# Performance work log

Measured on AMD Instinct MI355X. Metric: run time of the kernel, lower is better.

## Reference

```python
import jax, jax.numpy as jnp
import numpy as np
from jax import lax

D_MODEL = 256
SCALES = 3
DM2 = 2 * D_MODEL            # 512, inner d_model of each Mamba2
EXPAND = 2
D_INNER = EXPAND * DM2       # 1024
HEADDIM = 64                 # Mamba2 default
NHEADS = D_INNER // HEADDIM  # 16
DSTATE = 128
DCONV = 4
D_IN_PROJ = 2 * D_INNER + 2 * DSTATE + NHEADS  # 2320
CONV_CH = D_INNER + 2 * DSTATE                 # 1280


def layernorm(x, g, b, eps=1e-5):
    mu = x.mean(-1, keepdims=True)
    v = ((x - mu) ** 2).mean(-1, keepdims=True)
    return (x - mu) * lax.rsqrt(v + eps) * g + b


def mamba2(x, Win, convw, convb, dtb, Alog, Dh, normw, Wout):
    # x: [B, L, DM2]
    Bb, L, _ = x.shape
    zxbcdt = x @ Win                                   # [B, L, 2320]
    z = zxbcdt[..., :D_INNER]                          # gate branch
    xBC = zxbcdt[..., D_INNER:D_INNER + CONV_CH]       # [B, L, 1280]
    dt = jax.nn.softplus(zxbcdt[..., -NHEADS:] + dtb)  # [B, L, H]
    # causal depthwise conv1d over time
    xc = lax.conv_general_dilated(
        xBC.transpose(0, 2, 1), convw[:, None, :], (1,), [(DCONV - 1, 0)],
        feature_group_count=CONV_CH, dimension_numbers=('NCH', 'OIH', 'NCH'))
    xBC = jax.nn.silu(xc.transpose(0, 2, 1) + convb)
    xs = xBC[..., :D_INNER].reshape(Bb, L, NHEADS, HEADDIM)  # [B,L,H,P]
    Bm = xBC[..., D_INNER:D_INNER + DSTATE]                  # [B,L,N] (ngroups=1)
    Cm = xBC[..., D_INNER + DSTATE:]                         # [B,L,N]
    A = -jnp.exp(Alog)                                       # [H]
    dA = jnp.exp(dt * A)                                     # [B,L,H]

    def step(h, inp):
        dA_t, dt_t, x_t, B_t, C_t = inp
        h = dA_t[:, :, None, None] * h + jnp.einsum('bh,bhp,bn->bhpn', dt_t, x_t, B_t)
        return h, jnp.einsum('bhpn,bn->bhp', h, C_t)

    h0 = jnp.zeros((Bb, NHEADS, HEADDIM, DSTATE), x.dtype)
    _, ys = lax.scan(step, h0, (dA.transpose(1, 0, 2), dt.transpose(1, 0, 2),
                                xs.transpose(1, 0, 2, 3), Bm.transpose(1, 0, 2),
                                Cm.transpose(1, 0, 2)))
    y = ys.transpose(1, 0, 2, 3) + Dh[None, None, :, None] * xs   # skip term
    y = y.reshape(Bb, L, D_INNER)
    y = y * jax.nn.silu(z)                                        # gated RMSNorm
    y = y * lax.rsqrt((y * y).mean(-1, keepdims=True) + 1e-5) * normw
    return y @ Wout


def msfusion(x, Wp, bp, Wpre, bpre, lnpre_g, lnpre_b, Wpost, bpost, lnpost_g, lnpost_b,
             Win_f, convw_f, convb_f, dtb_f, Alog_f, Dh_f, normw_f, Wout_f,
             Win_b, convw_b, convb_b, dtb_b, Alog_b, Dh_b, normw_b, Wout_b):
    B, S, T, D = x.shape
    x_ = x.transpose(0, 2, 1, 3).reshape(B, T, S * D)
    x_ = x_ @ Wp + bp                                  # 1x1 conv == linear
    shortcut = x_
    h = layernorm(x_ @ Wpre + bpre, lnpre_g, lnpre_b)  # [B,T,512]
    gate = jax.nn.silu(h)
    out_f = mamba2(h, Win_f, convw_f, convb_f, dtb_f, Alog_f, Dh_f, normw_f, Wout_f)
    out_b = jnp.flip(mamba2(jnp.flip(h, 1), Win_b, convw_b, convb_b, dtb_b, Alog_b, Dh_b, normw_b, Wout_b), 1)
    out = layernorm((out_f * gate + out_b * gate) @ Wpost + bpost, lnpost_g, lnpost_b) + shortcut
    fn = out / jnp.maximum(jnp.linalg.norm(out, axis=-1, keepdims=True), 1e-12)
    attn = jnp.einsum('btd,bsd->bts', fn, fn)          # [B,T,T]
    return out, attn


def setup_inputs() -> dict:
    key = jax.random.key(0)
    ks = iter(jax.random.split(key, 40))
    n = lambda shape, s=0.02: (s * jax.random.normal(next(ks), shape)).astype(jnp.float32)
    B, S, T, D = 4, SCALES, 2048, D_MODEL
    inp = {
        'x': jax.random.normal(next(ks), (B, S, T, D), jnp.float32),
        'Wp': n((S * D, D)), 'bp': n((D,)),
        'Wpre': n((D, DM2)), 'bpre': n((DM2,)),
        'lnpre_g': jnp.ones((DM2,), jnp.float32), 'lnpre_b': jnp.zeros((DM2,), jnp.float32),
        'Wpost': n((DM2, D)), 'bpost': n((D,)),
        'lnpost_g': jnp.ones((D,), jnp.float32), 'lnpost_b': jnp.zeros((D,), jnp.float32),
    }
    for sfx in ('f', 'b'):
        inp['Win_' + sfx] = n((DM2, D_IN_PROJ))
        inp['convw_' + sfx] = n((CONV_CH, DCONV), 0.1)
        inp['convb_' + sfx] = jnp.zeros((CONV_CH,), jnp.float32)
        inp['dtb_' + sfx] = n((NHEADS,), 0.5)
        inp['Alog_' + sfx] = jnp.log(jnp.arange(1, NHEADS + 1, dtype=jnp.float32))
        inp['Dh_' + sfx] = jnp.ones((NHEADS,), jnp.float32)
        inp['normw_' + sfx] = jnp.ones((D_INNER,), jnp.float32)
        inp['Wout_' + sfx] = n((D_INNER, DM2))
    return inp


def reference(x, Wp, bp, Wpre, bpre, lnpre_g, lnpre_b, Wpost, bpost, lnpost_g, lnpost_b,
              Win_f, convw_f, convb_f, dtb_f, Alog_f, Dh_f, normw_f, Wout_f,
              Win_b, convw_b, convb_b, dtb_b, Alog_b, Dh_b, normw_b, Wout_b):
    return msfusion(x, Wp, bp, Wpre, bpre, lnpre_g, lnpre_b, Wpost, bpost, lnpost_g, lnpost_b,
                    Win_f, convw_f, convb_f, dtb_f, Alog_f, Dh_f, normw_f, Wout_f,
                    Win_b, convw_b, convb_b, dtb_b, Alog_b, Dh_b, normw_b, Wout_b)
```

## Files before the change

### kernel.cpp

```cpp
#include <hip/hip_runtime.h>
#include <math.h>

__device__ __forceinline__ float sigf(float v) { return 1.f / (1.f + __expf(-v)); }

__device__ __forceinline__ short f2bf(float f) {
  unsigned int u = __builtin_bit_cast(unsigned int, f);
  unsigned int r = (u + 0x7fffu + ((u >> 16) & 1u)) >> 16;
  return (short)r;
}
__device__ __forceinline__ float bf2f(short s) {
  unsigned int u = ((unsigned int)(unsigned short)s) << 16;
  return __builtin_bit_cast(float, u);
}

typedef short bf16x8 __attribute__((ext_vector_type(8)));
typedef float f32x4 __attribute__((ext_vector_type(4)));

__device__ __forceinline__ void async16(const short* g, short* l) {
  __builtin_amdgcn_global_load_lds(
      (const __attribute__((address_space(1))) unsigned int*)g,
      (__attribute__((address_space(3))) unsigned int*)l, 16, 0, 0);
}

template<bool BIAS, bool ACC>
__global__ __launch_bounds__(256) void gemm16_kernel(
    const short* __restrict__ A, const short* __restrict__ Bt,
    const float* __restrict__ bias, float* __restrict__ C,
    int M, int N, int K, int ldc,
    long long sAb, long long sBb, long long sCb)
{
  __shared__ short sm[2][2][128 * 32];
  const int tid = threadIdx.x;
  const int wave = tid >> 6;
  const int lane = tid & 63;
  const int m0 = blockIdx.x * 128;
  const int n0 = blockIdx.y * 128;
  const int bz = blockIdx.z;
  const short* Ab = A + (size_t)bz * sAb;
  const short* Bb = Bt + (size_t)bz * sBb;
  float* Cb = C + (size_t)bz * sCb;

  f32x4 acc[4][4] = {};

  const int isB = wave >> 1;
  const int half = wave & 1;
  const short* gsrc = isB ? Bb : Ab;
  const int tile_r0 = isB ? n0 : m0;
  const int lrow = lane >> 2;
  const int lk = (lane & 3) * 8;
  const short* gbase = gsrc + (size_t)(tile_r0 + half * 64 + lrow) * K + lk;
  short* lbase0 = &sm[0][isB][(half * 64) * 32];
  short* lbase1 = &sm[1][isB][(half * 64) * 32];

  const int wm = wave >> 1, wn = wave & 1;
  const int nt = K >> 5;

  auto STAGE = [&](int buf, int t) {
    const short* g0 = gbase + t * 32;
    short* l0 = buf ? lbase1 : lbase0;
#pragma unroll
    for (int c = 0; c < 4; c++)
      async16(g0 + (size_t)c * 16 * K, l0 + c * 512);
  };

  STAGE(0, 0);
  asm volatile("s_waitcnt vmcnt(0)" ::: "memory");
  __builtin_amdgcn_s_barrier();

  int cur = 0;
  for (int t = 0; t < nt; ++t) {
    if (t + 1 < nt) STAGE(cur ^ 1, t + 1);
    bf16x8 af[4], bfr[4];
#pragma unroll
    for (int mt = 0; mt < 4; mt++)
      af[mt] = *(bf16x8*)&sm[cur][0][(wm * 64 + mt * 16 + (lane & 15)) * 32 + (lane >> 4) * 8];
#pragma unroll
    for (int nn = 0; nn < 4; nn++)
      bfr[nn] = *(bf16x8*)&sm[cur][1][(wn * 64 + nn * 16 + (lane & 15)) * 32 + (lane >> 4) * 8];
#pragma unroll
    for (int mt = 0; mt < 4; mt++)
#pragma unroll
      for (int nn = 0; nn < 4; nn++)
        acc[mt][nn] = __builtin_amdgcn_mfma_f32_16x16x32_bf16(bfr[nn], af[mt], acc[mt][nn], 0, 0, 0);
    asm volatile("s_waitcnt vmcnt(0)" ::: "memory");
    __builtin_amdgcn_s_barrier();
    cur ^= 1;
  }
  const int mcol = lane & 15;
  const int nq = (lane >> 4) * 4;
#pragma unroll
  for (int mt = 0; mt < 4; mt++) {
    int row = m0 + wm * 64 + mt * 16 + mcol;
#pragma unroll
    for (int nn = 0; nn < 4; nn++) {
      int col = n0 + wn * 64 + nn * 16 + nq;
      if (col >= N) continue;
      float4 v = make_float4(acc[mt][nn][0], acc[mt][nn][1], acc[mt][nn][2], acc[mt][nn][3]);
      float* cp = Cb + (size_t)row * ldc + col;
      if (BIAS) {
        float4 bv = *(const float4*)(bias + col);
        v.x += bv.x; v.y += bv.y; v.z += bv.z; v.w += bv.w;
      }
      if (ACC) {
        float4 ov = *(const float4*)cp;
        v.x += ov.x; v.y += ov.y; v.z += ov.z; v.w += ov.w;
      }
      *(float4*)cp = v;
    }
  }
}

__global__ void tcast_kernel(const float* __restrict__ W, short* __restrict__ Wt,
                             int K, int N)
{
  __shared__ float tile[32][33];
  int n0 = blockIdx.x * 32, k0 = blockIdx.y * 32;
  int c = threadIdx.x & 31, r8 = threadIdx.x >> 5;
#pragma unroll
  for (int i = 0; i < 4; i++) {
    int r = r8 + i * 8;
    int n = n0 + c;
    tile[r][c] = (n < N) ? W[(size_t)(k0 + r) * N + n] : 0.f;
  }
  __syncthreads();
#pragma unroll
  for (int i = 0; i < 4; i++) {
    int r = r8 + i * 8;
    Wt[(size_t)(n0 + r) * K + k0 + c] = f2bf(tile[c][r]);
  }
}

__global__ void gather_cast_kernel(const float* __restrict__ x, short* __restrict__ Ag)
{
  int idx = blockIdx.x * 256 + threadIdx.x;
  int m = idx / 192;
  int g = idx - m * 192;
  int k = g * 4;
  int s = k >> 8, d = k & 255;
  int b = m >> 11, t = m & 2047;
  float4 v = *(const float4*)(x + ((size_t)((b * 3 + s) * 2048 + t) << 8) + d);
  *(short4*)(Ag + (size_t)m * 768 + k) = make_short4(f2bf(v.x), f2bf(v.y), f2bf(v.z), f2bf(v.w));
}

__global__ void cast_kernel(const float* __restrict__ in, short* __restrict__ out)
{
  size_t idx = (size_t)blockIdx.x * 256 + threadIdx.x;
  float4 v = *(const float4*)(in + idx * 4);
  *(short4*)(out + idx * 4) = make_short4(f2bf(v.x), f2bf(v.y), f2bf(v.z), f2bf(v.w));
}

__global__ void ln512_kernel(float* __restrict__ xio, const float* __restrict__ g,
                             const float* __restrict__ b, short* __restrict__ o16)
{
  const int row = blockIdx.x;
  const int lane = threadIdx.x;
  float* xr = xio + (size_t)row * 512;
  float4 v0 = *(float4*)(xr + lane * 4);
  float4 v1 = *(float4*)(xr + 256 + lane * 4);
  float sum = v0.x + v0.y + v0.z + v0.w + v1.x + v1.y + v1.z + v1.w;
#pragma unroll
  for (int o = 32; o >= 1; o >>= 1) sum += __shfl_xor(sum, o);
  const float mu = sum * (1.f / 512.f);
  float d[8] = {v0.x - mu, v0.y - mu, v0.z - mu, v0.w - mu,
                v1.x - mu, v1.y - mu, v1.z - mu, v1.w - mu};
  float vs = 0.f;
#pragma unroll
  for (int i = 0; i < 8; i++) vs += d[i] * d[i];
#pragma unroll
  for (int o = 32; o >= 1; o >>= 1) vs += __shfl_xor(vs, o);
  const float inv = rsqrtf(vs * (1.f / 512.f) + 1e-5f);
  float4 g0 = *(const float4*)(g + lane * 4);
  float4 g1 = *(const float4*)(g + 256 + lane * 4);
  float4 b0 = *(const float4*)(b + lane * 4);
  float4 b1 = *(const float4*)(b + 256 + lane * 4);
  v0.x = d[0] * inv * g0.x + b0.x; v0.y = d[1] * inv * g0.y + b0.y;
  v0.z = d[2] * inv * g0.z + b0.z; v0.w = d[3] * inv * g0.w + b0.w;
  v1.x = d[4] * inv * g1.x + b1.x; v1.y = d[5] * inv * g1.y + b1.y;
  v1.z = d[6] * inv * g1.z + b1.z; v1.w = d[7] * inv * g1.w + b1.w;
  *(float4*)(xr + lane * 4) = v0;
  *(float4*)(xr + 256 + lane * 4) = v1;
  short* orow = o16 + (size_t)row * 512;
  *(short4*)(orow + lane * 4) = make_short4(f2bf(v0.x), f2bf(v0.y), f2bf(v0.z), f2bf(v0.w));
  *(short4*)(orow + 256 + lane * 4) = make_short4(f2bf(v1.x), f2bf(v1.y), f2bf(v1.z), f2bf(v1.w));
}

__global__ void dtprep_kernel(const float* __restrict__ Z, const float* __restrict__ dtb,
                              const float* __restrict__ Alog,
                              float* __restrict__ dtv, float* __restrict__ ldA)
{
  int idx = blockIdx.x * 256 + threadIdx.x;
  int row = idx >> 4, hh = idx & 15;
  float raw = Z[(size_t)row * 2320 + 2304 + hh] + dtb[hh];
  float dt = raw > 20.f ? raw : log1pf(expf(raw));
  dtv[idx] = dt;
  ldA[idx] = -dt * expf(Alog[hh]);
}

__global__ void conv_kernel(const float* __restrict__ Z, const float* __restrict__ convw,
                            const float* __restrict__ convb, short* __restrict__ xcv, int dir)
{
  int row = blockIdx.x;
  int c = blockIdx.y * 256 + threadIdx.x;
  int t = row & 2047;
  size_t bbase = (size_t)(row - t) * 2320;
  float wv[4] = {convw[c * 4 + 0], convw[c * 4 + 1], convw[c * 4 + 2], convw[c * 4 + 3]};
  float acc = convb[c];
#pragma unroll
  for (int k = 0; k < 4; k++) {
    int ts = dir ? (t + 3 - k) : (t - 3 + k);
    if (ts >= 0 && ts < 2048)
      acc += wv[k] * Z[bbase + (size_t)ts * 2320 + 1024 + c];
  }
  xcv[(size_t)row * 1280 + c] = f2bf(acc * sigf(acc));
}

__global__ __launch_bounds__(256) void chunk_state_kernel(
    const short* __restrict__ xcv, const float* __restrict__ dtv,
    const float* __restrict__ ldA, short* __restrict__ Sbuf,
    float* __restrict__ Pbuf, int dir)
{
  __shared__ float sw[64];
  __shared__ short sXT[64 * 72];
  __shared__ short sBw[128 * 72];
  const int bh = blockIdx.x, ck = blockIdx.y;
  const int b = bh >> 4, h = bh & 15;
  const int tid = threadIdx.x;
  const int wave = tid >> 6, lane = tid & 63;

  if (tid < 64) {
    int tg = ck * 64 + tid;
    int tt = dir ? 2047 - tg : tg;
    size_t r = (size_t)(b * 2048 + tt) * 16 + h;
    float v = ldA[r];
#pragma unroll
    for (int o = 1; o < 64; o <<= 1) { float u = __shfl_up(v, o); if (tid >= o) v += u; }
    float tot = __shfl(v, 63);
    sw[tid] = __expf(tot - v) * dtv[r];
    if (tid == 63) Pbuf[bh * 32 + ck] = __expf(tot);
  }
  __syncthreads();
  for (int i4 = tid; i4 < 512; i4 += 256) {
    int s = i4 >> 3, p0 = (i4 & 7) * 8;
    int tg = ck * 64 + s; int tt = dir ? 2047 - tg : tg;
    bf16x8 xv = *(const bf16x8*)(xcv + (size_t)(b * 2048 + tt) * 1280 + h * 64 + p0);
#pragma unroll
    for (int j = 0; j < 8; j++) sXT[(p0 + j) * 72 + s] = xv[j];
  }
  for (int i4 = tid; i4 < 1024; i4 += 256) {
    int s = i4 >> 4, n0 = (i4 & 15) * 8;
    int tg = ck * 64 + s; int tt = dir ? 2047 - tg : tg;
    bf16x8 bv = *(const bf16x8*)(xcv + (size_t)(b * 2048 + tt) * 1280 + 1024 + n0);
    float w = sw[s];
#pragma unroll
    for (int j = 0; j < 8; j++) sBw[(n0 + j) * 72 + s] = f2bf(w * bf2f(bv[j]));
  }
  __syncthreads();

  const int mcol = lane & 15, kgrp = (lane >> 4) * 8;
  bf16x8 af[2];
#pragma unroll
  for (int kk = 0; kk < 2; kk++)
    af[kk] = *(bf16x8*)&sXT[(wave * 16 + mcol) * 72 + kk * 32 + kgrp];
  f32x4 acc[8] = {};
#pragma unroll
  for (int j = 0; j < 8; j++)
#pragma unroll
    for (int kk = 0; kk < 2; kk++) {
      bf16x8 bf = *(bf16x8*)&sBw[(j * 16 + mcol) * 72 + kk * 32 + kgrp];
      acc[j] = __builtin_amdgcn_mfma_f32_16x16x32_bf16(bf, af[kk], acc[j], 0, 0, 0);
    }
  short* Sp = Sbuf + ((size_t)(bh * 32 + ck) << 13);
  const int p = wave * 16 + mcol;
  const int nq = (lane >> 4) * 4;
#pragma unroll
  for (int j = 0; j < 8; j++) {
    *(short4*)(Sp + p * 128 + j * 16 + nq) = make_short4(
        f2bf(acc[j][0]), f2bf(acc[j][1]), f2bf(acc[j][2]), f2bf(acc[j][3]));
  }
}

__global__ void chunk_scan_kernel(short* __restrict__ Sbuf, const float* __restrict__ Pbuf)
{
  int idx = blockIdx.x * 256 + threadIdx.x;
  int bh = idx >> 12, pr = idx & 4095;
  float h0 = 0.f, h1 = 0.f;
  for (int ck = 0; ck < 32; ck++) {
    size_t off = ((size_t)(bh * 32 + ck) << 13) + pr * 2;
    unsigned int u = *(const unsigned int*)(Sbuf + off);
    float s0 = bf2f((short)(u & 0xffff));
    float s1 = bf2f((short)(u >> 16));
    float P = Pbuf[bh * 32 + ck];
    unsigned int w = (unsigned int)(unsigned short)f2bf(h0) |
                     ((unsigned int)(unsigned short)f2bf(h1) << 16);
    *(unsigned int*)(Sbuf + off) = w;
    h0 = P * h0 + s0;
    h1 = P * h1 + s1;
  }
}

__global__ __launch_bounds__(256) void chunk_out_kernel(
    const short* __restrict__ xcv, const float* __restrict__ dtv,
    const float* __restrict__ ldA, const short* __restrict__ Sbuf,
    const float* __restrict__ Dh, short* __restrict__ y, int dir)
{
  extern __shared__ short smem16[];
  short* sC  = smem16;
  short* sB  = sC + 64 * 136;
  short* sH  = sB + 64 * 136;
  short* sXT = sH + 64 * 136;
  short* sP  = sXT + 64 * 72;
  float* sL  = (float*)(sP + 64 * 72);
  float* sdt = sL + 64;

  const int bh = blockIdx.x, ck = blockIdx.y;
  const int b = bh >> 4, h = bh & 15;
  const int tid = threadIdx.x;
  const int wave = tid >> 6, lane = tid & 63;

  if (tid < 64) {
    int tg = ck * 64 + tid;
    int tt = dir ? 2047 - tg : tg;
    size_t r = (size_t)(b * 2048 + tt) * 16 + h;
    float v = ldA[r];
#pragma unroll
    for (int o = 1; o < 64; o <<= 1) { float u = __shfl_up(v, o); if (tid >= o) v += u; }
    sL[tid] = v;
    sdt[tid] = dtv[r];
  }
  for (int i4 = tid; i4 < 1024; i4 += 256) {
    int t = i4 >> 4, c8 = (i4 & 15) * 8;
    int tg = ck * 64 + t; int tt = dir ? 2047 - tg : tg;
    const short* rp = xcv + (size_t)(b * 2048 + tt) * 1280;
    *(bf16x8*)&sB[t * 136 + c8] = *(const bf16x8*)(rp + 1024 + c8);
    *(bf16x8*)&sC[t * 136 + c8] = *(const bf16x8*)(rp + 1152 + c8);
  }
  for (int i4 = tid; i4 < 512; i4 += 256) {
    int t = i4 >> 3, p0 = (i4 & 7) * 8;
    int tg = ck * 64 + t; int tt = dir ? 2047 - tg : tg;
    bf16x8 xv = *(const bf16x8*)(xcv + (size_t)(b * 2048 + tt) * 1280 + h * 64 + p0);
#pragma unroll
    for (int j = 0; j < 8; j++) sXT[(p0 + j) * 72 + t] = xv[j];
  }
  const short* Hp = Sbuf + ((size_t)(bh * 32 + ck) << 13);
  for (int i4 = tid; i4 < 1024; i4 += 256) {
    int p = i4 >> 4, c8 = (i4 & 15) * 8;
    *(bf16x8*)&sH[p * 136 + c8] = *(const bf16x8*)(Hp + p * 128 + c8);
  }
  __syncthreads();

  const int mcol = lane & 15;
  const int kgrp = (lane >> 4) * 8;
  const int trow = wave * 16 + mcol;
  const int sq = (lane >> 4) * 4;

  bf16x8 afC[4];
#pragma unroll
  for (int kk = 0; kk < 4; kk++)
    afC[kk] = *(bf16x8*)&sC[trow * 136 + kk * 32 + kgrp];

  f32x4 sacc[4] = {};
#pragma unroll
  for (int j = 0; j < 4; j++)
#pragma unroll
    for (int kk = 0; kk < 4; kk++) {
      bf16x8 bf = *(bf16x8*)&sB[(j * 16 + mcol) * 136 + kk * 32 + kgrp];
      sacc[j] = __builtin_amdgcn_mfma_f32_16x16x32_bf16(bf, afC[kk], sacc[j], 0, 0, 0);
    }

  const float Lt = sL[trow];
#pragma unroll
  for (int j = 0; j < 4; j++) {
    int s0 = j * 16 + sq;
    float vr[4];
#pragma unroll
    for (int r = 0; r < 4; r++) {
      int s = s0 + r;
      vr[r] = (trow >= s) ? sacc[j][r] * __expf(Lt - sL[s]) * sdt[s] : 0.f;
    }
    *(short4*)&sP[trow * 72 + s0] = make_short4(
        f2bf(vr[0]), f2bf(vr[1]), f2bf(vr[2]), f2bf(vr[3]));
  }
  __syncthreads();

  bf16x8 afP[2];
#pragma unroll
  for (int kk = 0; kk < 2; kk++)
    afP[kk] = *(bf16x8*)&sP[trow * 72 + kk * 32 + kgrp];
  f32x4 yacc[4] = {};
#pragma unroll
  for (int j = 0; j < 4; j++)
#pragma unroll
    for (int kk = 0; kk < 2; kk++) {
      bf16x8 bf = *(bf16x8*)&sXT[(j * 16 + mcol) * 72 + kk * 32 + kgrp];
      yacc[j] = __builtin_amdgcn_mfma_f32_16x16x32_bf16(bf, afP[kk], yacc[j], 0, 0, 0);
    }
  f32x4 y2[4] = {};
#pragma unroll
  for (int j = 0; j < 4; j++)
#pragma unroll
    for (int kk = 0; kk < 4; kk++) {
      bf16x8 bf = *(bf16x8*)&sH[(j * 16 + mcol) * 136 + kk * 32 + kgrp];
      y2[j] = __builtin_amdgcn_mfma_f32_16x16x32_bf16(bf, afC[kk], y2[j], 0, 0, 0);
    }

  const float dh = Dh[h];
  const float eL = __expf(Lt);
  const int tg = ck * 64 + trow;
  const int tt = dir ? 2047 - tg : tg;
  short* yrow = y + (size_t)(b * 2048 + tt) * 1024 + h * 64;
#pragma unroll
  for (int j = 0; j < 4; j++) {
    int p0 = j * 16 + sq;
    short o[4];
#pragma unroll
    for (int r = 0; r < 4; r++) {
      float xv = bf2f(sXT[(p0 + r) * 72 + trow]);
      o[r] = f2bf(yacc[j][r] + eL * y2[j][r] + dh * xv);
    }
    *(short4*)(yrow + p0) = make_short4(o[0], o[1], o[2], o[3]);
  }
}

__global__ void rms_kernel(short* __restrict__ y, const float* __restrict__ Z,
                           const float* __restrict__ normw)
{
  const int row = blockIdx.x;
  const int lane = threadIdx.x;
  short* yr = y + (size_t)row * 1024;
  const float* zr = Z + (size_t)row * 2320;
  float vals[16];
  float ss = 0.f;
#pragma unroll
  for (int jj = 0; jj < 4; jj++) {
    int off = jj * 256 + lane * 4;
    short4 yv = *(short4*)(yr + off);
    float4 zv = *(const float4*)(zr + off);
    float a0 = bf2f(yv.x) * (zv.x * sigf(zv.x));
    float a1 = bf2f(yv.y) * (zv.y * sigf(zv.y));
    float a2 = bf2f(yv.z) * (zv.z * sigf(zv.z));
    float a3 = bf2f(yv.w) * (zv.w * sigf(zv.w));
    vals[jj * 4 + 0] = a0; vals[jj * 4 + 1] = a1;
    vals[jj * 4 + 2] = a2; vals[jj * 4 + 3] = a3;
    ss += a0 * a0 + a1 * a1 + a2 * a2 + a3 * a3;
  }
#pragma unroll
  for (int o = 32; o >= 1; o >>= 1) ss += __shfl_xor(ss, o);
  const float scale = rsqrtf(ss * (1.f / 1024.f) + 1e-5f);
#pragma unroll
  for (int jj = 0; jj < 4; jj++) {
    int off = jj * 256 + lane * 4;
    float4 nw = *(const float4*)(normw + off);
    *(short4*)(yr + off) = make_short4(
        f2bf(vals[jj * 4 + 0] * scale * nw.x), f2bf(vals[jj * 4 + 1] * scale * nw.y),
        f2bf(vals[jj * 4 + 2] * scale * nw.z), f2bf(vals[jj * 4 + 3] * scale * nw.w));
  }
}

__global__ void combine_kernel(const float* __restrict__ od, const float* __restrict__ h,
                               short* __restrict__ ob)
{
  size_t idx = (size_t)blockIdx.x * 256 + threadIdx.x;
  float4 o = ((const float4*)od)[idx];
  float4 g = ((const float4*)h)[idx];
  o.x *= g.x * sigf(g.x);
  o.y *= g.y * sigf(g.y);
  o.z *= g.z * sigf(g.z);
  o.w *= g.w * sigf(g.w);
  *(short4*)(ob + idx * 4) = make_short4(f2bf(o.x), f2bf(o.y), f2bf(o.z), f2bf(o.w));
}

__global__ void lnshort_kernel(const float* __restrict__ v, const float* __restrict__ g,
                               const float* __restrict__ b, const float* __restrict__ shortcut,
                               float* __restrict__ out0, short* __restrict__ fn)
{
  const int row = blockIdx.x;
  const int lane = threadIdx.x;
  size_t base = (size_t)row * 256;
  float4 x = *(const float4*)(v + base + lane * 4);
  float sum = x.x + x.y + x.z + x.w;
#pragma unroll
  for (int o = 32; o >= 1; o >>= 1) sum += __shfl_xor(sum, o);
  const float mu = sum * (1.f / 256.f);
  float d[4] = {x.x - mu, x.y - mu, x.z - mu, x.w - mu};
  float vs = d[0] * d[0] + d[1] * d[1] + d[2] * d[2] + d[3] * d[3];
#pragma unroll
  for (int o = 32; o >= 1; o >>= 1) vs += __shfl_xor(vs, o);
  const float inv = rsqrtf(vs * (1.f / 256.f) + 1e-5f);
  float4 gg = *(const float4*)(g + lane * 4);
  float4 bb = *(const float4*)(b + lane * 4);
  float4 sc = *(const float4*)(shortcut + base + lane * 4);
  float4 o4;
  o4.x = d[0] * inv * gg.x + bb.x + sc.x;
  o4.y = d[1] * inv * gg.y + bb.y + sc.y;
  o4.z = d[2] * inv * gg.z + bb.z + sc.z;
  o4.w = d[3] * inv * gg.w + bb.w + sc.w;
  *(float4*)(out0 + base + lane * 4) = o4;
  float ns = o4.x * o4.x + o4.y * o4.y + o4.z * o4.z + o4.w * o4.w;
#pragma unroll
  for (int o = 32; o >= 1; o >>= 1) ns += __shfl_xor(ns, o);
  const float r = 1.f / fmaxf(sqrtf(ns), 1e-12f);
  *(short4*)(fn + base + lane * 4) =
      make_short4(f2bf(o4.x * r), f2bf(o4.y * r), f2bf(o4.z * r), f2bf(o4.w * r));
}

extern "C" void kernel_launch(void* const* d_in, const int* in_sizes, int n_in,
                              void* d_out, int out_size, void* d_ws, size_t ws_size,
                              hipStream_t stream)
{
  (void)in_sizes; (void)n_in; (void)out_size; (void)ws_size;
  const float* x        = (const float*)d_in[0];
  const float* Wp       = (const float*)d_in[1];
  const float* bp       = (const float*)d_in[2];
  const float* Wpre     = (const float*)d_in[3];
  const float* bpre     = (const float*)d_in[4];
  const float* lnpre_g  = (const float*)d_in[5];
  const float* lnpre_b  = (const float*)d_in[6];
  const float* Wpost    = (const float*)d_in[7];
  const float* bpost    = (const float*)d_in[8];
  const float* lnpost_g = (const float*)d_in[9];
  const float* lnpost_b = (const float*)d_in[10];

  float* ws   = (float*)d_ws;
  float* Zb   = ws;
  float* xcvr = Zb + 19005440;
  float* xc   = xcvr + 10485760;
  float* hbuf = xc + 2097152;
  short* hb16 = (short*)(hbuf + 4194304);
  float* yb16f= hbuf + 4194304 + 2097152;
  short* yb16 = (short*)yb16f;
  float* od   = yb16f + 4194304;
  float* dtv  = od + 4194304;
  float* ldA  = dtv + 131072;
  float* Pbuf = ldA + 131072;
  short* WinT = (short*)(Pbuf + 2048);
  short* WoutT= WinT + 1245184;

  short* xcv16  = (short*)xcvr;
  short* Ag16   = (short*)xcvr;
  short* WpT    = (short*)(xcvr + 3145728);
  short* xcb    = (short*)xcvr;
  short* WpreT  = (short*)(xcvr + 1048576);
  short* ob16   = (short*)xcvr;
  short* WpostT = (short*)(xcvr + 2097152);
  float* vbuf = yb16f;
  short* fn16 = (short*)(yb16f + 2097152);

  float* out0 = (float*)d_out;
  float* attn = out0 + 2097152;
  short* Sbuf16 = (short*)attn;

  tcast_kernel<<<dim3(8, 24), 256, 0, stream>>>(Wp, WpT, 768, 256);
  gather_cast_kernel<<<6144, 256, 0, stream>>>(x, Ag16);
  gemm16_kernel<true, false><<<dim3(64, 2), 256, 0, stream>>>(Ag16, WpT, bp, xc, 8192, 256, 768, 256, 0, 0, 0);
  cast_kernel<<<2048, 256, 0, stream>>>(xc, xcb);
  tcast_kernel<<<dim3(16, 8), 256, 0, stream>>>(Wpre, WpreT, 256, 512);
  gemm16_kernel<true, false><<<dim3(64, 4), 256, 0, stream>>>(xcb, WpreT, bpre, hbuf, 8192, 512, 256, 512, 0, 0, 0);
  ln512_kernel<<<8192, 64, 0, stream>>>(hbuf, lnpre_g, lnpre_b, hb16);

  for (int dir = 0; dir < 2; dir++) {
    const float* Win   = (const float*)d_in[11 + dir * 8];
    const float* convw = (const float*)d_in[12 + dir * 8];
    const float* convb = (const float*)d_in[13 + dir * 8];
    const float* dtb   = (const float*)d_in[14 + dir * 8];
    const float* Alog  = (const float*)d_in[15 + dir * 8];
    const float* Dh    = (const float*)d_in[16 + dir * 8];
    const float* normw = (const float*)d_in[17 + dir * 8];
    const float* Wout  = (const float*)d_in[18 + dir * 8];

    tcast_kernel<<<dim3(76, 16), 256, 0, stream>>>(Win, WinT, 512, 2320);
    tcast_kernel<<<dim3(16, 32), 256, 0, stream>>>(Wout, WoutT, 1024, 512);
    gemm16_kernel<false, false><<<dim3(64, 19), 256, 0, stream>>>(hb16, WinT, nullptr, Zb, 8192, 2320, 512, 2320, 0, 0, 0);
    dtprep_kernel<<<512, 256, 0, stream>>>(Zb, dtb, Alog, dtv, ldA);
    conv_kernel<<<dim3(8192, 5), 256, 0, stream>>>(Zb, convw, convb, xcv16, dir);
    chunk_state_kernel<<<dim3(64, 32), 256, 0, stream>>>(xcv16, dtv, ldA, Sbuf16, Pbuf, dir);
    chunk_scan_kernel<<<1024, 256, 0, stream>>>(Sbuf16, Pbuf);
    chunk_out_kernel<<<dim3(64, 32), 256, 71168, stream>>>(xcv16, dtv, ldA, Sbuf16, Dh, yb16, dir);
    rms_kernel<<<8192, 64, 0, stream>>>(yb16, Zb, normw);
    if (dir == 0)
      gemm16_kernel<false, false><<<dim3(64, 4), 256, 0, stream>>>(yb16, WoutT, nullptr, od, 8192, 512, 1024, 512, 0, 0, 0);
    else
      gemm16_kernel<false, true><<<dim3(64, 4), 256, 0, stream>>>(yb16, WoutT, nullptr, od, 8192, 512, 1024, 512, 0, 0, 0);
  }

  combine_kernel<<<4096, 256, 0, stream>>>(od, hbuf, ob16);
  tcast_kernel<<<dim3(8, 16), 256, 0, stream>>>(Wpost, WpostT, 512, 256);
  gemm16_kernel<true, false><<<dim3(64, 2), 256, 0, stream>>>(ob16, WpostT, bpost, vbuf, 8192, 256, 512, 256, 0, 0, 0);
  lnshort_kernel<<<8192, 64, 0, stream>>>(vbuf, lnpost_g, lnpost_b, xc, out0, fn16);
  gemm16_kernel<false, false><<<dim3(16, 16, 4), 256, 0, stream>>>(
      fn16, fn16, nullptr, attn, 2048, 2048, 256, 2048,
      (long long)2048 * 256, (long long)2048 * 256, (long long)2048 * 2048);
}
```

Baseline: 627.5 us.

## Triple-buffer GEMM LDS staging and XOR-swizzle LDS layout

The bf16 MFMA GEMM goes from double to triple buffering of its LDS tiles. It now prefetches two K-steps ahead and waits with vmcnt(4) instead of draining all loads, so global loads stay in flight across more MFMA work. The global-to-LDS copy source address and the LDS read address both get an XOR swizzle of the 8-element k-chunk, which is meant to reduce LDS bank conflicts on the fragment reads. LDS use grows by half, which can lower occupancy.

Measured after the change: 690.6 us. 1.1x slower.

```diff
diff --git a/kernel.cpp b/kernel.cpp
--- a/kernel.cpp
+++ b/kernel.cpp
@@ -29,7 +29,7 @@
     int M, int N, int K, int ldc,
     long long sAb, long long sBb, long long sCb)
 {
-  __shared__ short sm[2][2][128 * 32];
+  __shared__ short sm[3][2][128 * 32];
   const int tid = threadIdx.x;
   const int wave = tid >> 6;
   const int lane = tid & 63;
@@ -47,44 +47,54 @@
   const short* gsrc = isB ? Bb : Ab;
   const int tile_r0 = isB ? n0 : m0;
   const int lrow = lane >> 2;
-  const int lk = (lane & 3) * 8;
+  const int lk = (((lane & 3) ^ ((lane >> 3) & 3)) * 8);
   const short* gbase = gsrc + (size_t)(tile_r0 + half * 64 + lrow) * K + lk;
-  short* lbase0 = &sm[0][isB][(half * 64) * 32];
-  short* lbase1 = &sm[1][isB][(half * 64) * 32];
+  short* lb0 = &sm[0][isB][(half * 64) * 32];
+  short* lb1 = &sm[1][isB][(half * 64) * 32];
+  short* lb2 = &sm[2][isB][(half * 64) * 32];
 
   const int wm = wave >> 1, wn = wave & 1;
   const int nt = K >> 5;
 
   auto STAGE = [&](int buf, int t) {
     const short* g0 = gbase + t * 32;
-    short* l0 = buf ? lbase1 : lbase0;
+    short* l0 = buf == 0 ? lb0 : (buf == 1 ? lb1 : lb2);
 #pragma unroll
     for (int c = 0; c < 4; c++)
       async16(g0 + (size_t)c * 16 * K, l0 + c * 512);
   };
 
   STAGE(0, 0);
-  asm volatile("s_waitcnt vmcnt(0)" ::: "memory");
+  if (nt > 1) STAGE(1, 1);
+  if (nt > 1) asm volatile("s_waitcnt vmcnt(4)" ::: "memory");
+  else        asm volatile("s_waitcnt vmcnt(0)" ::: "memory");
   __builtin_amdgcn_s_barrier();
 
+  const int rs = (((lane >> 4) ^ ((lane >> 1) & 3)) * 8);
   int cur = 0;
   for (int t = 0; t < nt; ++t) {
-    if (t + 1 < nt) STAGE(cur ^ 1, t + 1);
+    const int nxt2 = cur >= 1 ? cur - 1 : 2;
+    if (t + 2 < nt) STAGE(nxt2, t + 2);
+    const short* smA = &sm[cur][0][0];
+    const short* smB = &sm[cur][1][0];
     bf16x8 af[4], bfr[4];
 #pragma unroll
     for (int mt = 0; mt < 4; mt++)
-      af[mt] = *(bf16x8*)&sm[cur][0][(wm * 64 + mt * 16 + (lane & 15)) * 32 + (lane >> 4) * 8];
+      af[mt] = *(bf16x8*)&smA[(wm * 64 + mt * 16 + (lane & 15)) * 32 + rs];
 #pragma unroll
     for (int nn = 0; nn < 4; nn++)
-      bfr[nn] = *(bf16x8*)&sm[cur][1][(wn * 64 + nn * 16 + (lane & 15)) * 32 + (lane >> 4) * 8];
+      bfr[nn] = *(bf16x8*)&smB[(wn * 64 + nn * 16 + (lane & 15)) * 32 + rs];
 #pragma unroll
     for (int mt = 0; mt < 4; mt++)
 #pragma unroll
       for (int nn = 0; nn < 4; nn++)
         acc[mt][nn] = __builtin_amdgcn_mfma_f32_16x16x32_bf16(bfr[nn], af[mt], acc[mt][nn], 0, 0, 0);
-    asm volatile("s_waitcnt vmcnt(0)" ::: "memory");
-    __builtin_amdgcn_s_barrier();
-    cur ^= 1;
+    if (t + 1 < nt) {
+      if (t + 2 < nt) asm volatile("s_waitcnt vmcnt(4)" ::: "memory");
+      else            asm volatile("s_waitcnt vmcnt(0)" ::: "memory");
+      __builtin_amdgcn_s_barrier();
+    }
+    cur = cur >= 2 ? 0 : cur + 1;
   }
   const int mcol = lane & 15;
   const int nq = (lane >> 4) * 4;
```
